# Kernel tuning notes

Measured on AMD Instinct MI355X. Metric: run time of the kernel, lower is better.

The kernel has to match this reference:

```python
import jax, jax.numpy as jnp
import numpy as np

DIM = 768
NUM_HEADS = 24
WS = 8
SHIFT = 4
HID = 3072
HW = 96
EPS = 1e-5


def _rel_pos_index(ws):
    coords = np.stack(np.meshgrid(np.arange(ws), np.arange(ws), indexing='ij')).reshape(2, -1)
    rel = (coords[:, :, None] - coords[:, None, :]).transpose(1, 2, 0) + (ws - 1)
    rel[:, :, 0] *= 2 * ws - 1
    return rel.sum(-1).reshape(-1)  # (N*N,)


def _shift_mask(Hp, Wp, ws, shift):
    img = np.zeros((Hp, Wp))
    cnt = 0
    for hs in (slice(0, -ws), slice(-ws, -shift), slice(-shift, None)):
        for wsl in (slice(0, -ws), slice(-ws, -shift), slice(-shift, None)):
            img[hs, wsl] = cnt
            cnt += 1
    mw = img.reshape(Hp // ws, ws, Wp // ws, ws).transpose(0, 2, 1, 3).reshape(-1, ws * ws)
    diff = mw[:, None, :] - mw[:, :, None]
    return jnp.asarray(np.where(diff != 0, -100.0, 0.0), dtype=jnp.float32)  # (nW, N, N)


_REL_IDX = jnp.asarray(_rel_pos_index(WS))
_MASK = _shift_mask(HW, HW, WS, SHIFT)


def setup_inputs() -> dict:
    key = jax.random.key(0)
    ks = jax.random.split(key, 8)
    s = 0.02
    return {
        'x_chw': jax.random.normal(ks[0], (DIM, HW, HW), jnp.float32),
        'norm1_w': jnp.ones((DIM,), jnp.float32),
        'norm1_b': jnp.zeros((DIM,), jnp.float32),
        'qkv_w': jax.random.normal(ks[1], (3 * DIM, DIM), jnp.float32) * s,
        'qkv_b': jnp.zeros((3 * DIM,), jnp.float32),
        'proj_w': jax.random.normal(ks[2], (DIM, DIM), jnp.float32) * s,
        'proj_b': jnp.zeros((DIM,), jnp.float32),
        'bias_table': jax.random.normal(ks[3], ((2 * WS - 1) ** 2, NUM_HEADS), jnp.float32),
        'norm2_w': jnp.ones((DIM,), jnp.float32),
        'norm2_b': jnp.zeros((DIM,), jnp.float32),
        'fc1_w': jax.random.normal(ks[4], (HID, DIM), jnp.float32) * s,
        'fc1_b': jnp.zeros((HID,), jnp.float32),
        'fc2_w': jax.random.normal(ks[5], (DIM, HID), jnp.float32) * s,
        'fc2_b': jnp.zeros((DIM,), jnp.float32),
    }


def _ln_chw(x, g, b):
    # LayerNorm over channel axis at each spatial location; x: (C,H,W)
    mu = x.mean(axis=0, keepdims=True)
    var = x.var(axis=0, keepdims=True)
    return (x - mu) * jax.lax.rsqrt(var + EPS) * g[:, None, None] + b[:, None, None]


def reference(x_chw, norm1_w, norm1_b, qkv_w, qkv_b, proj_w, proj_b, bias_table,
              norm2_w, norm2_b, fc1_w, fc1_b, fc2_w, fc2_b):
    C, H, W = x_chw.shape
    Hh, dh, N = NUM_HEADS, C // NUM_HEADS, WS * WS
    scale = 1.0 / np.sqrt(dh)

    x_norm = _ln_chw(x_chw, norm1_w, norm1_b)
    x_shift = jnp.roll(x_norm, shift=(-SHIFT, -SHIFT), axis=(1, 2))
    x_hwc = jnp.moveaxis(x_shift, 0, -1)  # (H,W,C); H,W divisible by WS -> no pad

    nWh, nWw = H // WS, W // WS
    xw = x_hwc.reshape(nWh, WS, nWw, WS, C).transpose(0, 2, 1, 3, 4).reshape(nWh * nWw, N, C)

    qkv = xw @ qkv_w.T + qkv_b  # (nW, N, 3C)
    q, k, v = jnp.split(qkv, 3, axis=-1)

    def to_heads(t):
        return t.reshape(-1, N, Hh, dh).transpose(0, 2, 1, 3)  # (nW, Hh, N, dh)

    q, k, v = to_heads(q), to_heads(k), to_heads(v)
    attn = jnp.einsum('whnd,whmd->whnm', q * scale, k)
    bias = bias_table[_REL_IDX].reshape(N, N, Hh).transpose(2, 0, 1)  # (Hh, N, N)
    attn = attn + bias[None] + _MASK[:, None, :, :]
    attn = jax.nn.softmax(attn, axis=-1)
    out = jnp.einsum('whnm,whmd->whnd', attn, v)
    out = out.transpose(0, 2, 1, 3).reshape(-1, N, C)
    out = out @ proj_w.T + proj_b

    x_hwc = out.reshape(nWh, nWw, WS, WS, C).transpose(0, 2, 1, 3, 4).reshape(H, W, C)
    x_merge = jnp.moveaxis(x_hwc, -1, 0)
    x_merge = jnp.roll(x_merge, shift=(SHIFT, SHIFT), axis=(1, 2))

    x = x_chw + x_merge
    x2 = _ln_chw(x, norm2_w, norm2_b)
    tok = jnp.moveaxis(x2, 0, -1).reshape(H * W, C)
    tok = jax.nn.gelu(tok @ fc1_w.T + fc1_b) @ fc2_w.T + fc2_b
    x2 = jnp.moveaxis(tok.reshape(H, W, C), -1, 0)
    return x + x2
```

## Files before the change

### kernel.cpp

```cpp
#include <hip/hip_runtime.h>
#include <hip/hip_bf16.h>


typedef __attribute__((ext_vector_type(8))) short bf16x8;
typedef __attribute__((ext_vector_type(4))) float f32x4;

__device__ __forceinline__ short f2bf(float f){
  unsigned u = __builtin_bit_cast(unsigned, f);
  unsigned r = (u + 0x7FFFu + ((u >> 16) & 1u)) >> 16;
  return (short)r;
}
__device__ __forceinline__ float bf2f(short s){
  unsigned u = ((unsigned)(unsigned short)s) << 16;
  return __builtin_bit_cast(float, u);
}
__device__ __forceinline__ float gelu_tanh(float v){
  const float c = 0.7978845608028654f;
  float u = c * (v + 0.044715f * v * v * v);
  float e = __expf(2.f * u);
  float th = 1.f - 2.f / (e + 1.f);
  return 0.5f * v * (1.f + th);
}
__device__ __forceinline__ void gl2lds16(const short* g, short* l){
  __builtin_amdgcn_global_load_lds(
      (const __attribute__((address_space(1))) int*)g,
      (__attribute__((address_space(3))) int*)l, 16, 0, 0);
}

__global__ void k_f2b(const float* __restrict__ in, short* __restrict__ out, int n){
  int i = blockIdx.x * 256 + threadIdx.x;
  if (i < n) out[i] = f2bf(in[i]);
}

__global__ void k_bias_pre(const float* __restrict__ btab, float* __restrict__ biasp){
  int idx = blockIdx.x * 256 + threadIdx.x;
  int h = idx >> 12, mn = idx & 4095, m = mn >> 6, n = mn & 63;
  int i1 = m >> 3, j1 = m & 7, i2 = n >> 3, j2 = n & 7;
  biasp[idx] = btab[((i1 - i2 + 7) * 15 + (j1 - j2 + 7)) * 24 + h];
}

__global__ void k_ln_stats(const float* __restrict__ x, float* __restrict__ sums,
                           float* __restrict__ sumsq){
  const int p = blockIdx.x * 256 + threadIdx.x;
  const int c0 = blockIdx.y * 64;
  float s = 0.f, s2 = 0.f;
  for (int c = c0; c < c0 + 64; ++c){
    float v = x[(long)c * 9216 + p];
    s += v; s2 += v * v;
  }
  atomicAdd(&sums[p], s);
  atomicAdd(&sumsq[p], s2);
}
__global__ void k_ln_fin(const float* __restrict__ sums, const float* __restrict__ sumsq,
                         float* __restrict__ mean, float* __restrict__ rstd){
  const int p = blockIdx.x * 256 + threadIdx.x;
  float m = sums[p] * (1.f / 768.f);
  float v = sumsq[p] * (1.f / 768.f) - m * m;
  mean[p] = m;
  rstd[p] = rsqrtf(v + 1e-5f);
}

__global__ void k_ln1_win(const float* __restrict__ x, const float* __restrict__ mean,
                          const float* __restrict__ rstd, const float* __restrict__ g,
                          const float* __restrict__ b, short* __restrict__ tok){
  __shared__ float tile[64][65];
  const int w = blockIdx.x, ct = blockIdx.y * 64;
  const int wh = w / 12, ww = w - wh * 12;
  const int t = threadIdx.x;
  for (int e = t; e < 4096; e += 256){
    const int cl = e >> 6, pix = e & 63;
    int pr = wh * 8 + (pix >> 3) + 4; if (pr >= 96) pr -= 96;
    int pc = ww * 8 + (pix & 7) + 4;  if (pc >= 96) pc -= 96;
    tile[pix][cl] = x[(long)(ct + cl) * 9216 + pr * 96 + pc];
  }
  __syncthreads();
  for (int e = t; e < 4096; e += 256){
    const int pix = e >> 6, cl = e & 63;
    int pr = wh * 8 + (pix >> 3) + 4; if (pr >= 96) pr -= 96;
    int pc = ww * 8 + (pix & 7) + 4;  if (pc >= 96) pc -= 96;
    const int p = pr * 96 + pc;
    float v = (tile[pix][cl] - mean[p]) * rstd[p] * g[ct + cl] + b[ct + cl];
    tok[(long)(w * 64 + pix) * 768 + ct + cl] = f2bf(v);
  }
}

__global__ void k_merge_win(const float* __restrict__ x, const short* __restrict__ ptok,
                            float* __restrict__ x1){
  __shared__ float tile[64][65];
  const int w = blockIdx.x, ct = blockIdx.y * 64;
  const int wh = w / 12, ww = w - wh * 12;
  const int t = threadIdx.x;
  for (int e = t; e < 4096; e += 256){
    const int pix = e >> 6, cl = e & 63;
    tile[pix][cl] = bf2f(ptok[(long)(w * 64 + pix) * 768 + ct + cl]);
  }
  __syncthreads();
  for (int e = t; e < 4096; e += 256){
    const int cl = e >> 6, pix = e & 63;
    int pr = wh * 8 + (pix >> 3) + 4; if (pr >= 96) pr -= 96;
    int pc = ww * 8 + (pix & 7) + 4;  if (pc >= 96) pc -= 96;
    const long gi = (long)(ct + cl) * 9216 + pr * 96 + pc;
    x1[gi] = x[gi] + tile[pix][cl];
  }
}

__global__ void k_ln2_raster(const float* __restrict__ x1, const float* __restrict__ mean,
                             const float* __restrict__ rstd, const float* __restrict__ g,
                             const float* __restrict__ b, short* __restrict__ tok){
  __shared__ float tile[96][65];
  const int hrow = blockIdx.x, ct = blockIdx.y * 64;
  const int t = threadIdx.x;
  for (int e = t; e < 6144; e += 256){
    const int cl = e / 96, p = e - cl * 96;
    tile[p][cl] = x1[(long)(ct + cl) * 9216 + hrow * 96 + p];
  }
  __syncthreads();
  for (int e = t; e < 6144; e += 256){
    const int p = e >> 6, cl = e & 63;
    const int gp = hrow * 96 + p;
    float v = (tile[p][cl] - mean[gp]) * rstd[gp] * g[ct + cl] + b[ct + cl];
    tok[(long)gp * 768 + ct + cl] = f2bf(v);
  }
}

__global__ void k_merge_raster(const float* __restrict__ x1, const short* __restrict__ mtok,
                               float* __restrict__ out){
  __shared__ float tile[96][65];
  const int hrow = blockIdx.x, ct = blockIdx.y * 64;
  const int t = threadIdx.x;
  for (int e = t; e < 6144; e += 256){
    const int p = e >> 6, cl = e & 63;
    tile[p][cl] = bf2f(mtok[(long)(hrow * 96 + p) * 768 + ct + cl]);
  }
  __syncthreads();
  for (int e = t; e < 6144; e += 256){
    const int cl = e / 96, p = e - cl * 96;
    const long gi = (long)(ct + cl) * 9216 + hrow * 96 + p;
    out[gi] = x1[gi] + tile[p][cl];
  }
}

__global__ __launch_bounds__(256) void k_gemm_bt(
    const short* __restrict__ A, const short* __restrict__ B,
    const float* __restrict__ bias, short* __restrict__ C,
    int N, int K, int do_gelu)
{
  __shared__ short Al[2][4096];
  __shared__ short Bl[2][4096];
  const int tid = threadIdx.x;
  const int wave = tid >> 6, lane = tid & 63;
  const int l15 = lane & 15, lg = lane >> 4;
  const int bn = blockIdx.x, bm = blockIdx.y;
  const long Abase = (long)bm * 128 * K;
  const long Bbase = (long)bn * 128 * K;
  const int srow = tid >> 2;
  const int scol = (tid & 3) << 3;
  const int wr = (wave >> 1) * 64, wc = (wave & 1) * 64;

  f32x4 acc[4][4] = {};

  auto stage = [&](int buf, int k0){
    const short* gA = A + Abase + (long)srow * K + k0 + scol;
    const short* gB = B + Bbase + (long)srow * K + k0 + scol;
    short* lA = &Al[buf][wave * 512];
    short* lB = &Bl[buf][wave * 512];
    gl2lds16(gA, lA);
    gl2lds16(gA + (long)64 * K, lA + 2048);
    gl2lds16(gB, lB);
    gl2lds16(gB + (long)64 * K, lB + 2048);
  };

  const int NKT = K >> 5;
  int buf = 0;
  stage(0, 0);
  for (int kt = 0; kt < NKT; ++kt){
    if (kt + 1 < NKT) stage(buf ^ 1, (kt + 1) << 5);
    __syncthreads();
    bf16x8 af[4], bfv[4];
    #pragma unroll
    for (int m = 0; m < 4; ++m)
      af[m] = *(const bf16x8*)&Al[buf][(wr + m * 16 + l15) * 32 + lg * 8];
    #pragma unroll
    for (int n2 = 0; n2 < 4; ++n2)
      bfv[n2] = *(const bf16x8*)&Bl[buf][(wc + n2 * 16 + l15) * 32 + lg * 8];
    #pragma unroll
    for (int m = 0; m < 4; ++m)
      #pragma unroll
      for (int n2 = 0; n2 < 4; ++n2)
        acc[m][n2] = __builtin_amdgcn_mfma_f32_16x16x32_bf16(af[m], bfv[n2], acc[m][n2], 0, 0, 0);
    __syncthreads();
    buf ^= 1;
  }

  const long row0 = (long)bm * 128 + wr + lg * 4;
  const int col0 = bn * 128 + wc + l15;
  #pragma unroll
  for (int m = 0; m < 4; ++m){
    #pragma unroll
    for (int n2 = 0; n2 < 4; ++n2){
      const int col = col0 + n2 * 16;
      const float bb = bias[col];
      #pragma unroll
      for (int r = 0; r < 4; ++r){
        float v = acc[m][n2][r] + bb;
        if (do_gelu) v = gelu_tanh(v);
        C[(row0 + m * 16 + r) * (long)N + col] = f2bf(v);
      }
    }
  }
}

#define PSTR 72
__global__ __launch_bounds__(256) void k_attn_mfma(
    const short* __restrict__ qkv, const float* __restrict__ biasp,
    short* __restrict__ out)
{
  __shared__ short Pl[4][64 * PSTR];
  const int tid = threadIdx.x, wv = tid >> 6, lane = tid & 63;
  const int l15 = lane & 15, lg = lane >> 4;
  const int task = blockIdx.x * 4 + wv;
  const int w = task / 24, h = task - w * 24;
  const int wh = w / 12, ww = w - wh * 12;
  const long base = (long)w * 64 * 2304;
  const float scale = 0.17677669529663687f;

  bf16x8 qf[4], kf[4];
  #pragma unroll
  for (int mi = 0; mi < 4; ++mi)
    qf[mi] = *(const bf16x8*)(qkv + base + (long)(mi * 16 + l15) * 2304 + h * 32 + lg * 8);
  #pragma unroll
  for (int ni = 0; ni < 4; ++ni)
    kf[ni] = *(const bf16x8*)(qkv + base + (long)(ni * 16 + l15) * 2304 + 768 + h * 32 + lg * 8);

  f32x4 acc[4][4] = {};
  #pragma unroll
  for (int mi = 0; mi < 4; ++mi)
    #pragma unroll
    for (int ni = 0; ni < 4; ++ni)
      acc[mi][ni] = __builtin_amdgcn_mfma_f32_16x16x32_bf16(qf[mi], kf[ni], acc[mi][ni], 0, 0, 0);

  const float* bh = biasp + h * 4096;
  #pragma unroll
  for (int mi = 0; mi < 4; ++mi){
    #pragma unroll
    for (int r = 0; r < 4; ++r){
      const int m = mi * 16 + lg * 4 + r;
      const int i1 = m >> 3, j1 = m & 7;
      const int labm = ((wh == 11) ? ((i1 >= 4) ? 2 : 1) : 0) * 3
                     + ((ww == 11) ? ((j1 >= 4) ? 2 : 1) : 0);
      #pragma unroll
      for (int ni = 0; ni < 4; ++ni){
        const int n = ni * 16 + l15;
        const int i2 = n >> 3, j2 = n & 7;
        const int labn = ((wh == 11) ? ((i2 >= 4) ? 2 : 1) : 0) * 3
                       + ((ww == 11) ? ((j2 >= 4) ? 2 : 1) : 0);
        float s = acc[mi][ni][r] * scale + bh[m * 64 + n];
        if (labm != labn) s -= 100.f;
        acc[mi][ni][r] = s;
      }
    }
  }

  float inv[4][4];
  #pragma unroll
  for (int mi = 0; mi < 4; ++mi){
    #pragma unroll
    for (int r = 0; r < 4; ++r){
      float mx = fmaxf(fmaxf(acc[mi][0][r], acc[mi][1][r]),
                       fmaxf(acc[mi][2][r], acc[mi][3][r]));
      #pragma unroll
      for (int off = 1; off < 16; off <<= 1) mx = fmaxf(mx, __shfl_xor(mx, off));
      float sum = 0.f;
      #pragma unroll
      for (int ni = 0; ni < 4; ++ni){
        float e = __expf(acc[mi][ni][r] - mx);
        acc[mi][ni][r] = e;
        sum += e;
      }
      #pragma unroll
      for (int off = 1; off < 16; off <<= 1) sum += __shfl_xor(sum, off);
      inv[mi][r] = 1.f / sum;
    }
  }

  short* pw = &Pl[wv][0];
  #pragma unroll
  for (int mi = 0; mi < 4; ++mi)
    #pragma unroll
    for (int ni = 0; ni < 4; ++ni)
      #pragma unroll
      for (int r = 0; r < 4; ++r)
        pw[(mi * 16 + lg * 4 + r) * PSTR + ni * 16 + l15] = f2bf(acc[mi][ni][r]);
  __syncthreads();

  f32x4 acc2[4][2] = {};
  #pragma unroll
  for (int kk = 0; kk < 2; ++kk){
    bf16x8 pa[4], vb[2];
    #pragma unroll
    for (int mi = 0; mi < 4; ++mi)
      pa[mi] = *(const bf16x8*)&pw[(mi * 16 + l15) * PSTR + kk * 32 + lg * 8];
    #pragma unroll
    for (int dj = 0; dj < 2; ++dj){
      bf16x8 t;
      #pragma unroll
      for (int e = 0; e < 8; ++e)
        t[e] = qkv[base + (long)(kk * 32 + lg * 8 + e) * 2304 + 1536 + h * 32 + dj * 16 + l15];
      vb[dj] = t;
    }
    #pragma unroll
    for (int mi = 0; mi < 4; ++mi)
      #pragma unroll
      for (int dj = 0; dj < 2; ++dj)
        acc2[mi][dj] = __builtin_amdgcn_mfma_f32_16x16x32_bf16(pa[mi], vb[dj], acc2[mi][dj], 0, 0, 0);
  }

  #pragma unroll
  for (int mi = 0; mi < 4; ++mi){
    #pragma unroll
    for (int r = 0; r < 4; ++r){
      const int m = mi * 16 + lg * 4 + r;
      const long ob = (long)(w * 64 + m) * 768 + h * 32;
      #pragma unroll
      for (int dj = 0; dj < 2; ++dj)
        out[ob + dj * 16 + l15] = f2bf(acc2[mi][dj][r] * inv[mi][r]);
    }
  }
}

extern "C" void kernel_launch(void* const* d_in, const int* in_sizes, int n_in,
                              void* d_out, int out_size, void* d_ws, size_t ws_size,
                              hipStream_t stream)
{
  const float* x      = (const float*)d_in[0];
  const float* n1w    = (const float*)d_in[1];
  const float* n1b    = (const float*)d_in[2];
  const float* qkv_w  = (const float*)d_in[3];
  const float* qkv_b  = (const float*)d_in[4];
  const float* proj_w = (const float*)d_in[5];
  const float* proj_b = (const float*)d_in[6];
  const float* btab   = (const float*)d_in[7];
  const float* n2w    = (const float*)d_in[8];
  const float* n2b    = (const float*)d_in[9];
  const float* fc1_w  = (const float*)d_in[10];
  const float* fc1_b  = (const float*)d_in[11];
  const float* fc2_w  = (const float*)d_in[12];
  const float* fc2_b  = (const float*)d_in[13];
  float* out = (float*)d_out;
  char* ws = (char*)d_ws;

  short* WQ   = (short*)(ws + 0);
  short* WP   = (short*)(ws + 3538944);
  short* W1   = (short*)(ws + 4718592);
  short* W2   = (short*)(ws + 9437184);
  float* SUMS = (float*)(ws + 14155776);
  float* SUMSQ= (float*)(ws + 14192640);
  float* MEAN = (float*)(ws + 14229504);
  float* RSTD = (float*)(ws + 14266368);
  float* BIASP= (float*)(ws + 14303232);
  short* TOK  = (short*)(ws + 14696448);
  short* BIG  = (short*)(ws + 28852224);
  short* ATT  = (short*)(ws + 85475328);
  short* PRJ  = (short*)(ws + 99631104);
  float* X1   = (float*)(ws + 113786880);

  k_f2b<<<(2304 * 768 + 255) / 256, 256, 0, stream>>>(qkv_w, WQ, 2304 * 768);
  k_f2b<<<(768 * 768 + 255) / 256, 256, 0, stream>>>(proj_w, WP, 768 * 768);
  k_f2b<<<(3072 * 768 + 255) / 256, 256, 0, stream>>>(fc1_w, W1, 3072 * 768);
  k_f2b<<<(768 * 3072 + 255) / 256, 256, 0, stream>>>(fc2_w, W2, 768 * 3072);
  k_bias_pre<<<(24 * 4096) / 256, 256, 0, stream>>>(btab, BIASP);

  hipMemsetAsync(SUMS, 0, 2 * 9216 * 4, stream);
  k_ln_stats<<<dim3(36, 12), 256, 0, stream>>>(x, SUMS, SUMSQ);
  k_ln_fin<<<36, 256, 0, stream>>>(SUMS, SUMSQ, MEAN, RSTD);
  k_ln1_win<<<dim3(144, 12), 256, 0, stream>>>(x, MEAN, RSTD, n1w, n1b, TOK);

  k_gemm_bt<<<dim3(18, 72), 256, 0, stream>>>(TOK, WQ, qkv_b, BIG, 2304, 768, 0);
  k_attn_mfma<<<864, 256, 0, stream>>>(BIG, BIASP, ATT);
  k_gemm_bt<<<dim3(6, 72), 256, 0, stream>>>(ATT, WP, proj_b, PRJ, 768, 768, 0);
  k_merge_win<<<dim3(144, 12), 256, 0, stream>>>(x, PRJ, X1);

  hipMemsetAsync(SUMS, 0, 2 * 9216 * 4, stream);
  k_ln_stats<<<dim3(36, 12), 256, 0, stream>>>(X1, SUMS, SUMSQ);
  k_ln_fin<<<36, 256, 0, stream>>>(SUMS, SUMSQ, MEAN, RSTD);
  k_ln2_raster<<<dim3(96, 12), 256, 0, stream>>>(X1, MEAN, RSTD, n2w, n2b, TOK);

  k_gemm_bt<<<dim3(24, 72), 256, 0, stream>>>(TOK, W1, fc1_b, BIG, 3072, 768, 1);
  k_gemm_bt<<<dim3(6, 72), 256, 0, stream>>>(BIG, W2, fc2_b, ATT, 768, 3072, 0);
  k_merge_raster<<<dim3(96, 12), 256, 0, stream>>>(X1, ATT, out);
}
```

Baseline: 515.9 us.

## Add 256x256-tile 8-wave GEMM with phased LDS prefetch for QKV and FC1

Adds a new bf16 MFMA GEMM kernel that uses 256x256 output tiles, 512 threads and a 128KB double-buffered LDS with an XOR swizzle. Each K step is split into four phases that interleave LDS fragment reads, async global-to-LDS prefetch of the next tile and MFMA bursts raised with s_setprio. The QKV and FC1 GEMMs now use this kernel instead of the 128x128 one. The larger tiles are meant to raise arithmetic intensity and overlap loads with compute. In exchange there are fewer blocks (324 and 432), which may leave the 256 CUs poorly balanced, and register pressure rises.

```diff
diff --git a/kernel.cpp b/kernel.cpp
--- a/kernel.cpp
+++ b/kernel.cpp
@@ -205,6 +205,120 @@
         float v = acc[m][n2][r] + bb;
         if (do_gelu) v = gelu_tanh(v);
         C[(row0 + m * 16 + r) * (long)N + col] = f2bf(v);
+      }
+    }
+  }
+}
+
+__global__ __launch_bounds__(512, 2) void k_gemm256(
+    const short* __restrict__ A, const short* __restrict__ B,
+    const float* __restrict__ bias, short* __restrict__ C,
+    int N, int K, int do_gelu)
+{
+  __shared__ short sm[65536];
+  const int tid = threadIdx.x;
+  const int w = tid >> 6, l = tid & 63;
+  const int l15 = l & 15, lg = l >> 4;
+  const int wm = w >> 2, wn = w & 3;
+  const int bn = blockIdx.x, bm = blockIdx.y;
+  const int xorb = l15 & 7;
+
+  const int srow = w * 8 + (l >> 3);
+  const int scol = ((l & 7) ^ (l >> 3)) << 3;
+  const long arow0 = (long)bm * 256, brow0 = (long)bn * 256;
+
+  f32x4 acc[8][4] = {};
+
+  auto stageH = [&](int p, int o, int H, int k0){
+    const short* gb = (o ? B + (brow0 + H * 128 + srow) * (long)K
+                         : A + (arow0 + H * 128 + srow) * (long)K) + k0 + scol;
+    short* lb = &sm[(p * 2 + o) * 16384 + H * 8192 + w * 512];
+    gl2lds16(gb, lb);
+    gl2lds16(gb + (long)64 * K, lb + 4096);
+  };
+
+  stageH(0, 1, 0, 0); stageH(0, 1, 1, 0); stageH(0, 0, 0, 0); stageH(0, 0, 1, 0);
+
+  const int NT = K >> 6;
+  for (int t = 0; t < NT; ++t){
+    const int p = t & 1;
+    const int k1 = (t + 1) << 6;
+    const bool pre = (t + 1 < NT);
+    const int ab = (p * 2) * 16384, bb = (p * 2 + 1) * 16384;
+    bf16x8 bfr[8];
+
+#define PHASE_MFMA(f0)                                                          \
+    __builtin_amdgcn_s_setprio(1);                                              \
+    _Pragma("unroll")                                                           \
+    for (int fi = 0; fi < 2; ++fi)                                              \
+      _Pragma("unroll")                                                         \
+      for (int nf = 0; nf < 4; ++nf)                                            \
+        _Pragma("unroll")                                                       \
+        for (int ks = 0; ks < 2; ++ks)                                          \
+          acc[(f0) + fi][nf] = __builtin_amdgcn_mfma_f32_16x16x32_bf16(         \
+              afr[fi][ks], bfr[nf * 2 + ks], acc[(f0) + fi][nf], 0, 0, 0);      \
+    __builtin_amdgcn_s_setprio(0);
+
+#define PHASE_AREAD(f0)                                                         \
+    bf16x8 afr[2][2];                                                           \
+    _Pragma("unroll")                                                           \
+    for (int fi = 0; fi < 2; ++fi){                                             \
+      const int ra = (((f0) + fi) * 32 + wm * 16 + l15) * 64;                   \
+      _Pragma("unroll")                                                         \
+      for (int ks = 0; ks < 2; ++ks)                                            \
+        afr[fi][ks] = *(const bf16x8*)&sm[ab + ra + (((ks * 4 + lg) ^ xorb) << 3)]; \
+    }
+
+    asm volatile("s_waitcnt vmcnt(2)" ::: "memory");
+    __builtin_amdgcn_s_barrier();
+    {
+      #pragma unroll
+      for (int nf = 0; nf < 4; ++nf){
+        const int rb = (wn * 64 + nf * 16 + l15) * 64;
+        #pragma unroll
+        for (int ks = 0; ks < 2; ++ks)
+          bfr[nf * 2 + ks] = *(const bf16x8*)&sm[bb + rb + (((ks * 4 + lg) ^ xorb) << 3)];
+      }
+      PHASE_AREAD(0)
+      if (pre) stageH(p ^ 1, 1, 0, k1);
+      PHASE_MFMA(0)
+    }
+    __builtin_amdgcn_s_barrier();
+    {
+      PHASE_AREAD(2)
+      if (pre) stageH(p ^ 1, 1, 1, k1);
+      PHASE_MFMA(2)
+    }
+    if (pre) asm volatile("s_waitcnt vmcnt(4)" ::: "memory");
+    else     asm volatile("s_waitcnt vmcnt(0)" ::: "memory");
+    __builtin_amdgcn_s_barrier();
+    {
+      PHASE_AREAD(4)
+      if (pre) stageH(p ^ 1, 0, 0, k1);
+      PHASE_MFMA(4)
+    }
+    __builtin_amdgcn_s_barrier();
+    {
+      PHASE_AREAD(6)
+      if (pre) stageH(p ^ 1, 0, 1, k1);
+      PHASE_MFMA(6)
+    }
+#undef PHASE_MFMA
+#undef PHASE_AREAD
+  }
+
+  #pragma unroll
+  for (int fr = 0; fr < 8; ++fr){
+    const long row0 = (long)bm * 256 + fr * 32 + wm * 16 + lg * 4;
+    #pragma unroll
+    for (int nf = 0; nf < 4; ++nf){
+      const int col = bn * 256 + wn * 64 + nf * 16 + l15;
+      const float bb2 = bias[col];
+      #pragma unroll
+      for (int r = 0; r < 4; ++r){
+        float v = acc[fr][nf][r] + bb2;
+        if (do_gelu) v = gelu_tanh(v);
+        C[(row0 + r) * (long)N + col] = f2bf(v);
       }
     }
   }
@@ -375,7 +489,7 @@
   k_ln_fin<<<36, 256, 0, stream>>>(SUMS, SUMSQ, MEAN, RSTD);
   k_ln1_win<<<dim3(144, 12), 256, 0, stream>>>(x, MEAN, RSTD, n1w, n1b, TOK);
 
-  k_gemm_bt<<<dim3(18, 72), 256, 0, stream>>>(TOK, WQ, qkv_b, BIG, 2304, 768, 0);
+  k_gemm256<<<dim3(9, 36), 512, 0, stream>>>(TOK, WQ, qkv_b, BIG, 2304, 768, 0);
   k_attn_mfma<<<864, 256, 0, stream>>>(BIG, BIASP, ATT);
   k_gemm_bt<<<dim3(6, 72), 256, 0, stream>>>(ATT, WP, proj_b, PRJ, 768, 768, 0);
   k_merge_win<<<dim3(144, 12), 256, 0, stream>>>(x, PRJ, X1);
@@ -385,7 +499,7 @@
   k_ln_fin<<<36, 256, 0, stream>>>(SUMS, SUMSQ, MEAN, RSTD);
   k_ln2_raster<<<dim3(96, 12), 256, 0, stream>>>(X1, MEAN, RSTD, n2w, n2b, TOK);
 
-  k_gemm_bt<<<dim3(24, 72), 256, 0, stream>>>(TOK, W1, fc1_b, BIG, 3072, 768, 1);
+  k_gemm256<<<dim3(12, 36), 512, 0, stream>>>(TOK, W1, fc1_b, BIG, 3072, 768, 1);
   k_gemm_bt<<<dim3(6, 72), 256, 0, stream>>>(BIG, W2, fc2_b, ATT, 768, 3072, 0);
   k_merge_raster<<<dim3(96, 12), 256, 0, stream>>>(X1, ATT, out);
 }
```

Result: no change. 507.1 us (-1.7%).

## Swizzle GEMM block mapping across XCDs and replace syncthreads with explicit waits

Applied to the files above, without the earlier changes.

The GEMM grid becomes 1D, and block indices are remapped so that consecutive tiles land on the same XCD. Tiles sharing A or B operands then reuse the same L2. The double-buffer loop drops one of its two __syncthreads per iteration in favour of explicit vmcnt and lgkmcnt waits plus a single s_barrier, with a sched_barrier before the MFMAs. This is meant to cut barrier overhead and improve L2 hit rates. It risks ordering hazards if the global-to-LDS loads are not fully covered by the vmcnt wait.

```diff
diff --git a/kernel.cpp b/kernel.cpp
--- a/kernel.cpp
+++ b/kernel.cpp
@@ -143,14 +143,20 @@
 __global__ __launch_bounds__(256) void k_gemm_bt(
     const short* __restrict__ A, const short* __restrict__ B,
     const float* __restrict__ bias, short* __restrict__ C,
-    int N, int K, int do_gelu)
+    int N, int K, int NBN, int do_gelu)
 {
   __shared__ short Al[2][4096];
   __shared__ short Bl[2][4096];
   const int tid = threadIdx.x;
   const int wave = tid >> 6, lane = tid & 63;
   const int l15 = lane & 15, lg = lane >> 4;
-  const int bn = blockIdx.x, bm = blockIdx.y;
+
+  const int nb = gridDim.x;
+  const int q = nb >> 3, r = nb & 7;
+  const int xcd = blockIdx.x & 7, loc = blockIdx.x >> 3;
+  const int swz = (xcd < r ? xcd * (q + 1) : r * (q + 1) + (xcd - r) * q) + loc;
+  const int bn = swz % NBN, bm = swz / NBN;
+
   const long Abase = (long)bm * 128 * K;
   const long Bbase = (long)bn * 128 * K;
   const int srow = tid >> 2;
@@ -171,11 +177,13 @@
   };
 
   const int NKT = K >> 5;
+  stage(0, 0);
+  asm volatile("s_waitcnt vmcnt(0)" ::: "memory");
+  __builtin_amdgcn_s_barrier();
+
   int buf = 0;
-  stage(0, 0);
   for (int kt = 0; kt < NKT; ++kt){
     if (kt + 1 < NKT) stage(buf ^ 1, (kt + 1) << 5);
-    __syncthreads();
     bf16x8 af[4], bfv[4];
     #pragma unroll
     for (int m = 0; m < 4; ++m)
@@ -183,12 +191,15 @@
     #pragma unroll
     for (int n2 = 0; n2 < 4; ++n2)
       bfv[n2] = *(const bf16x8*)&Bl[buf][(wc + n2 * 16 + l15) * 32 + lg * 8];
+    asm volatile("s_waitcnt lgkmcnt(0)" ::: "memory");
+    __builtin_amdgcn_sched_barrier(0);
     #pragma unroll
     for (int m = 0; m < 4; ++m)
       #pragma unroll
       for (int n2 = 0; n2 < 4; ++n2)
         acc[m][n2] = __builtin_amdgcn_mfma_f32_16x16x32_bf16(af[m], bfv[n2], acc[m][n2], 0, 0, 0);
-    __syncthreads();
+    asm volatile("s_waitcnt vmcnt(0)" ::: "memory");
+    __builtin_amdgcn_s_barrier();
     buf ^= 1;
   }
 
@@ -201,10 +212,10 @@
       const int col = col0 + n2 * 16;
       const float bb = bias[col];
       #pragma unroll
-      for (int r = 0; r < 4; ++r){
-        float v = acc[m][n2][r] + bb;
+      for (int r2 = 0; r2 < 4; ++r2){
+        float v = acc[m][n2][r2] + bb;
         if (do_gelu) v = gelu_tanh(v);
-        C[(row0 + m * 16 + r) * (long)N + col] = f2bf(v);
+        C[(row0 + m * 16 + r2) * (long)N + col] = f2bf(v);
       }
     }
   }
@@ -375,9 +386,9 @@
   k_ln_fin<<<36, 256, 0, stream>>>(SUMS, SUMSQ, MEAN, RSTD);
   k_ln1_win<<<dim3(144, 12), 256, 0, stream>>>(x, MEAN, RSTD, n1w, n1b, TOK);
 
-  k_gemm_bt<<<dim3(18, 72), 256, 0, stream>>>(TOK, WQ, qkv_b, BIG, 2304, 768, 0);
+  k_gemm_bt<<<18 * 72, 256, 0, stream>>>(TOK, WQ, qkv_b, BIG, 2304, 768, 18, 0);
   k_attn_mfma<<<864, 256, 0, stream>>>(BIG, BIASP, ATT);
-  k_gemm_bt<<<dim3(6, 72), 256, 0, stream>>>(ATT, WP, proj_b, PRJ, 768, 768, 0);
+  k_gemm_bt<<<6 * 72, 256, 0, stream>>>(ATT, WP, proj_b, PRJ, 768, 768, 6, 0);
   k_merge_win<<<dim3(144, 12), 256, 0, stream>>>(x, PRJ, X1);
 
   hipMemsetAsync(SUMS, 0, 2 * 9216 * 4, stream);
@@ -385,7 +396,7 @@
   k_ln_fin<<<36, 256, 0, stream>>>(SUMS, SUMSQ, MEAN, RSTD);
   k_ln2_raster<<<dim3(96, 12), 256, 0, stream>>>(X1, MEAN, RSTD, n2w, n2b, TOK);
 
-  k_gemm_bt<<<dim3(24, 72), 256, 0, stream>>>(TOK, W1, fc1_b, BIG, 3072, 768, 1);
-  k_gemm_bt<<<dim3(6, 72), 256, 0, stream>>>(BIG, W2, fc2_b, ATT, 768, 3072, 0);
+  k_gemm_bt<<<24 * 72, 256, 0, stream>>>(TOK, W1, fc1_b, BIG, 3072, 768, 24, 1);
+  k_gemm_bt<<<6 * 72, 256, 0, stream>>>(BIG, W2, fc2_b, ATT, 768, 3072, 6, 0);
   k_merge_raster<<<dim3(96, 12), 256, 0, stream>>>(X1, ATT, out);
 }
```

Measured after the change: 502.3 us. 2.6% less time.
